# Performance work log

Hardware: AMD Instinct MI355X
Metric: run time of the kernel (lower is better)

## Reference

```python
import jax, jax.numpy as jnp
import numpy as np

S, B, V = 128, 64, 32000
EH, EO, H, O = 512, 512, 1024, 1024
THRESH = 1e-06


def _thresh(x):
    # nn.Threshold(1e-6, 0): x if x > 1e-6 else 0
    return jnp.where(x > THRESH, x, 0.0)


def setup_inputs() -> dict:
    key = jax.random.key(0)
    ks = jax.random.split(key, 12)
    ids = jax.random.randint(ks[0], (S, B), 0, V, dtype=jnp.int32)
    s = 0.02
    return {
        "ids": ids,
        "W1": jax.random.normal(ks[1], (EH, V), jnp.float32) * s,
        "b1": jax.random.normal(ks[2], (EH,), jnp.float32) * s,
        "W2": jax.random.normal(ks[3], (EO, EH), jnp.float32) * s,
        "b2": jax.random.normal(ks[4], (EO,), jnp.float32) * s,
        "W_ih": jax.random.normal(ks[5], (3 * H, EO), jnp.float32) * s,
        "b_ih": jax.random.normal(ks[6], (3 * H,), jnp.float32) * s,
        "W_hh": jax.random.normal(ks[7], (3 * H, H), jnp.float32) * s,
        "b_hh": jax.random.normal(ks[8], (3 * H,), jnp.float32) * s,
        "W_out": jax.random.normal(ks[9], (O, H), jnp.float32) * s,
        "b_out": jax.random.normal(ks[10], (O,), jnp.float32) * s,
    }


def reference(ids, W1, b1, W2, b2, W_ih, b_ih, W_hh, b_hh, W_out, b_out):
    # one_hot(ids, V) @ W1.T + b1 == exact gather of W1 columns (sum of zeros is exact)
    emb = _thresh(jnp.take(W1.T, ids, axis=0) + b1)            # [S, B, EH]
    x = _thresh(jnp.einsum('sbe,oe->sbo', emb, W2) + b2)       # [S, B, EO]
    # Precompute all input-gate projections in one GEMM
    xW = jnp.einsum('sbe,ge->sbg', x, W_ih) + b_ih             # [S, B, 3H]

    def step(h, xw):
        gh = h @ W_hh.T + b_hh                                 # [B, 3H]
        xr, xz, xn = jnp.split(xw, 3, axis=-1)
        hr, hz, hn = jnp.split(gh, 3, axis=-1)
        r = jax.nn.sigmoid(xr + hr)
        z = jax.nn.sigmoid(xz + hz)
        n = jnp.tanh(xn + r * hn)
        h_new = (1.0 - z) * n + z * h
        return h_new, None

    h0 = jnp.zeros((B, H), dtype=x.dtype)
    hT, _ = jax.lax.scan(step, h0, xW)                         # [B, H]
    # Dropout is identity in inference; final Linear
    out = hT @ W_out.T + b_out                                 # [B, O]
    return out[None]                                           # [1, B, O] (h_n layout)
```

## Files before the change

### kernel.cpp

```cpp
#include <hip/hip_runtime.h>
#include <stdint.h>
#include <stddef.h>

#define S_LEN 128
#define B_SZ  64
#define V_SZ  32000
#define EH    512
#define EO    512
#define H_SZ  1024
#define O_SZ  1024
#define G3    3072

typedef __attribute__((ext_vector_type(8))) short short8;
typedef __attribute__((ext_vector_type(4))) float floatx4;
typedef __attribute__((ext_vector_type(8))) unsigned short ushortx8;
typedef __attribute__((ext_vector_type(4))) unsigned uintx4;

__device__ __forceinline__ unsigned short f2bf(float f) {
  unsigned u = __builtin_bit_cast(unsigned, f);
  u += 0x7FFFu + ((u >> 16) & 1u);
  return (unsigned short)(u >> 16);
}
__device__ __forceinline__ float bf2f(unsigned short h) {
  unsigned u = ((unsigned)h) << 16;
  return __builtin_bit_cast(float, u);
}

__device__ __forceinline__ void gld_lds16(const void* g, void* l) {
  __builtin_amdgcn_global_load_lds((const __attribute__((address_space(1))) void*)g,
                                   (__attribute__((address_space(3))) void*)l, 16, 0, 0);
}

__global__ __launch_bounds__(256) void cvt_bf16(const float* __restrict__ in,
                                                unsigned short* __restrict__ out, int n4) {
  int i = blockIdx.x * 256 + threadIdx.x;
  if (i < n4) {
    float4 v = ((const float4*)in)[i];
    ushort4 o;
    o.x = f2bf(v.x); o.y = f2bf(v.y); o.z = f2bf(v.z); o.w = f2bf(v.w);
    ((ushort4*)out)[i] = o;
  }
}

__global__ __launch_bounds__(256) void transpose_w1_bf16(const float* __restrict__ W1,
                                                         unsigned short* __restrict__ W1T) {
  __shared__ unsigned short tile[64][72];
  int t = threadIdx.x;
  int v0 = blockIdx.x * 64;
  int e0 = blockIdx.y * 64;
  for (int i = 0; i < 4; ++i) {
    int e = (t >> 4) + i * 16;
    int v = (t & 15) * 4;
    float4 w = *(const float4*)&W1[(size_t)(e0 + e) * V_SZ + v0 + v];
    tile[v + 0][e] = f2bf(w.x);
    tile[v + 1][e] = f2bf(w.y);
    tile[v + 2][e] = f2bf(w.z);
    tile[v + 3][e] = f2bf(w.w);
  }
  __syncthreads();
  for (int i = 0; i < 2; ++i) {
    int v = (t >> 3) + i * 32;
    int e = (t & 7) * 8;
    ushortx8 o;
    for (int j = 0; j < 8; ++j) o[j] = tile[v][e + j];
    *(ushortx8*)&W1T[(size_t)(v0 + v) * EH + e0 + e] = o;
  }
}

__global__ __launch_bounds__(256) void gather_emb(const int* __restrict__ ids,
                                                  const unsigned short* __restrict__ W1T,
                                                  const float* __restrict__ b1,
                                                  unsigned short* __restrict__ emb) {
  int t = threadIdx.x;
  int tok = blockIdx.x * 4 + (t >> 6);
  int lane = t & 63;
  int id = ids[tok];
  ushortx8 w = *(const ushortx8*)&W1T[(size_t)id * EH + lane * 8];
  float4 blo = *(const float4*)&b1[lane * 8];
  float4 bhi = *(const float4*)&b1[lane * 8 + 4];
  float bv[8] = {blo.x, blo.y, blo.z, blo.w, bhi.x, bhi.y, bhi.z, bhi.w};
  ushortx8 o;
  for (int j = 0; j < 8; ++j) {
    float x = bf2f(w[j]) + bv[j];
    x = (x > 1e-6f) ? x : 0.0f;
    o[j] = f2bf(x);
  }
  *(ushortx8*)&emb[(size_t)tok * EH + lane * 8] = o;
}

template <int ACT, int OUT_BF16>
__global__ __launch_bounds__(256) void gemm_bt(const unsigned short* __restrict__ A,
                                               const unsigned short* __restrict__ B,
                                               const float* __restrict__ bias,
                                               void* __restrict__ Cout,
                                               int M, int N, int K) {
  __shared__ unsigned short lA[128 * 32];
  __shared__ unsigned short lB[128 * 32];
  int t = threadIdx.x;
  int lane = t & 63;
  int wave = t >> 6;
  int bn = blockIdx.x, bm = blockIdx.y;
  int wm = (wave >> 1) * 64;
  int wn = (wave & 1) * 64;
  floatx4 acc[4][4] = {};

  int arow = t >> 2;
  int acol = (t & 3) * 8;

  int ga0 = bm * 128 + arow;       if (ga0 >= M) ga0 = M - 1;
  int ga1 = bm * 128 + arow + 64;  if (ga1 >= M) ga1 = M - 1;
  const unsigned short* a0 = A + (size_t)ga0 * K + acol;
  const unsigned short* a1 = A + (size_t)ga1 * K + acol;
  const unsigned short* b0 = B + (size_t)(bn * 128 + arow) * K + acol;
  const unsigned short* b1 = B + (size_t)(bn * 128 + arow + 64) * K + acol;
  unsigned short* lA0 = &lA[t * 8];
  unsigned short* lA1 = &lA[t * 8 + 64 * 32];
  unsigned short* lB0 = &lB[t * 8];
  unsigned short* lB1 = &lB[t * 8 + 64 * 32];

  for (int k0 = 0; k0 < K; k0 += 32) {
    __syncthreads();
    gld_lds16(a0 + k0, lA0);
    gld_lds16(a1 + k0, lA1);
    gld_lds16(b0 + k0, lB0);
    gld_lds16(b1 + k0, lB1);
    __syncthreads();
    short8 af[4], bfr[4];
    for (int i = 0; i < 4; ++i)
      af[i] = *(const short8*)&lA[(wm + i * 16 + (lane & 15)) * 32 + (lane >> 4) * 8];
    for (int j = 0; j < 4; ++j)
      bfr[j] = *(const short8*)&lB[(wn + j * 16 + (lane & 15)) * 32 + (lane >> 4) * 8];
    for (int i = 0; i < 4; ++i)
      for (int j = 0; j < 4; ++j)
        acc[i][j] = __builtin_amdgcn_mfma_f32_16x16x32_bf16(af[i], bfr[j], acc[i][j], 0, 0, 0);
  }

  int rowq = (lane >> 4) * 4;
  for (int j = 0; j < 4; ++j) {
    int col = bn * 128 + wn + j * 16 + (lane & 15);
    float bv = bias[col];
    for (int i = 0; i < 4; ++i) {
      int row0 = bm * 128 + wm + i * 16 + rowq;
      for (int r = 0; r < 4; ++r) {
        int row = row0 + r;
        if (row < M) {
          float v = acc[i][j][r] + bv;
          if (ACT) v = (v > 1e-6f) ? v : 0.0f;
          if (OUT_BF16) ((unsigned short*)Cout)[(size_t)row * N + col] = f2bf(v);
          else          ((float*)Cout)[(size_t)row * N + col] = v;
        }
      }
    }
  }
}

__global__ __launch_bounds__(256) void prep_whh(const float* __restrict__ W_hh,
                                                unsigned short* __restrict__ Wprep) {
  int tid = blockIdx.x * 256 + threadIdx.x;
  int lane = tid & 63;
  int c = tid >> 6;
  int cg = c / 96;
  int r  = c % 96;
  int g  = r >> 5;
  int t  = r & 31;
  int row = g * H_SZ + cg * 16 + (lane & 15);
  int k   = t * 32 + (lane >> 4) * 8;
  const float* src = &W_hh[(size_t)row * H_SZ + k];
  float4 v0 = *(const float4*)src;
  float4 v1 = *(const float4*)(src + 4);
  ushortx8 o;
  o[0] = f2bf(v0.x); o[1] = f2bf(v0.y); o[2] = f2bf(v0.z); o[3] = f2bf(v0.w);
  o[4] = f2bf(v1.x); o[5] = f2bf(v1.y); o[6] = f2bf(v1.z); o[7] = f2bf(v1.w);
  ((ushortx8*)Wprep)[tid] = o;
}

__global__ __launch_bounds__(256) void gru_persist(const unsigned short* __restrict__ hprep0,
                                                   unsigned short* __restrict__ hprep1,
                                                   unsigned short* __restrict__ hbfinal,
                                                   const unsigned short* __restrict__ Wprep,
                                                   const float* __restrict__ b_hh,
                                                   const unsigned short* __restrict__ xW,
                                                   unsigned* __restrict__ bar) {
  __shared__ unsigned short lB[96 * 512];
  __shared__ float lgh[3][4][256];
  __shared__ float lhf[256];
  int t = threadIdx.x;
  int lane = t & 63;
  int w = t >> 6;
  int bg = blockIdx.x >> 6;
  int cg = blockIdx.x & 63;

  const unsigned short* wsrc = Wprep + (size_t)cg * 96 * 512;
  for (int i = 0; i < 24; ++i) {
    int c = w * 24 + i;
    gld_lds16(wsrc + (size_t)c * 512 + lane * 8, &lB[c * 512 + lane * 8]);
  }
  lhf[t] = 0.0f;

  int b_loc = t >> 4;
  int j_loc = t & 15;
  int jcol = cg * 16 + j_loc;
  int bglob = bg * 16 + b_loc;
  float bhr = b_hh[jcol];
  float bhz = b_hh[H_SZ + jcol];
  float bhn = b_hh[2 * H_SZ + jcol];
  int tt2 = jcol >> 5;
  int q   = (jcol >> 3) & 3;
  int jj  = jcol & 7;
  int Ls  = b_loc | (q << 4);
  size_t hw_off32 = ((((size_t)(bg * 32 + tt2) * 64 + Ls) * 8) + (jj & ~1)) >> 1;

  const unsigned short* hbufs[2] = {hprep0, hprep1};
  unsigned* barp = bar + bg * 64;
  __syncthreads();

  for (int s = 0; s < S_LEN; ++s) {
    const unsigned short* hr = hbufs[s & 1];
    unsigned* hw32 = (unsigned*)hbufs[(s + 1) & 1];

    uintx4 av[8];
#pragma unroll
    for (int i = 0; i < 8; ++i) {
      int tt = w * 8 + i;
      const void* ap = hr + ((size_t)(bg * 32 + tt) * 64 + lane) * 8;
      asm volatile("global_load_dwordx4 %0, %1, off sc1" : "=v"(av[i]) : "v"(ap));
    }
    const unsigned short* xs = xW + (size_t)s * B_SZ * G3 + (size_t)bglob * G3;
    float xr = bf2f(xs[jcol]);
    float xz = bf2f(xs[H_SZ + jcol]);
    float xn = bf2f(xs[2 * H_SZ + jcol]);
    asm volatile("s_waitcnt vmcnt(0)"
                 : "+v"(av[0]), "+v"(av[1]), "+v"(av[2]), "+v"(av[3]),
                   "+v"(av[4]), "+v"(av[5]), "+v"(av[6]), "+v"(av[7])
                 :: "memory");

    floatx4 acc[3] = {};
#pragma unroll
    for (int i = 0; i < 8; ++i) {
      int tt = w * 8 + i;
      short8 a = __builtin_bit_cast(short8, av[i]);
#pragma unroll
      for (int g = 0; g < 3; ++g) {
        short8 bfr = *(const short8*)&lB[((g * 32 + tt) * 64 + lane) * 8];
        acc[g] = __builtin_amdgcn_mfma_f32_16x16x32_bf16(a, bfr, acc[g], 0, 0, 0);
      }
    }
#pragma unroll
    for (int g = 0; g < 3; ++g)
#pragma unroll
      for (int r = 0; r < 4; ++r)
        lgh[g][w][((lane >> 4) * 4 + r) * 16 + (lane & 15)] = acc[g][r];
    __syncthreads();

    float ghr = lgh[0][0][t] + lgh[0][1][t] + lgh[0][2][t] + lgh[0][3][t] + bhr;
    float ghz = lgh[1][0][t] + lgh[1][1][t] + lgh[1][2][t] + lgh[1][3][t] + bhz;
    float ghn = lgh[2][0][t] + lgh[2][1][t] + lgh[2][2][t] + lgh[2][3][t] + bhn;
    float rr = 1.0f / (1.0f + __expf(-(xr + ghr)));
    float zz = 1.0f / (1.0f + __expf(-(xz + ghz)));
    float nn = tanhf(xn + rr * ghn);
    float ho = lhf[t];
    float hnew = (1.0f - zz) * nn + zz * ho;
    lhf[t] = hnew;

    unsigned hb = (unsigned)f2bf(hnew);
    unsigned other = (unsigned)__shfl_xor((int)hb, 1);
    if ((jj & 1) == 0) {
      unsigned packed = hb | (other << 16);
      __hip_atomic_store(hw32 + hw_off32, packed,
                         __ATOMIC_RELAXED, __HIP_MEMORY_SCOPE_AGENT);
    }
    if (s == S_LEN - 1) hbfinal[(size_t)bglob * H_SZ + jcol] = (unsigned short)hb;

    if (s < S_LEN - 1) {
      __syncthreads();
      if (t == 0) {
        __hip_atomic_fetch_add(barp, 1u, __ATOMIC_RELAXED, __HIP_MEMORY_SCOPE_AGENT);
        unsigned target = 64u * (unsigned)(s + 1);
        while (__hip_atomic_load(barp, __ATOMIC_RELAXED, __HIP_MEMORY_SCOPE_AGENT) < target)
          __builtin_amdgcn_s_sleep(2);
      }
      __syncthreads();
    }
  }
}

extern "C" void kernel_launch(void* const* d_in, const int* in_sizes, int n_in,
                              void* d_out, int out_size, void* d_ws, size_t ws_size,
                              hipStream_t stream) {
  const int*   ids   = (const int*)d_in[0];
  const float* W1    = (const float*)d_in[1];
  const float* b1    = (const float*)d_in[2];
  const float* W2    = (const float*)d_in[3];
  const float* b2    = (const float*)d_in[4];
  const float* W_ih  = (const float*)d_in[5];
  const float* b_ih  = (const float*)d_in[6];
  const float* W_hh  = (const float*)d_in[7];
  const float* b_hh  = (const float*)d_in[8];
  const float* W_out = (const float*)d_in[9];
  const float* b_out = (const float*)d_in[10];
  float* out = (float*)d_out;

  uint8_t* wsp = (uint8_t*)d_ws;
  auto alloc = [&](size_t bytes) {
    uint8_t* p = wsp;
    wsp += (bytes + 255) & ~(size_t)255;
    return p;
  };
  unsigned short* W1T   = (unsigned short*)alloc((size_t)V_SZ * EH * 2);
  unsigned short* W2b   = (unsigned short*)alloc((size_t)EO * EH * 2);
  unsigned short* Wihb  = (unsigned short*)alloc((size_t)G3 * EO * 2);
  unsigned short* Wprep = (unsigned short*)alloc((size_t)G3 * H_SZ * 2);
  unsigned short* Woutb = (unsigned short*)alloc((size_t)O_SZ * H_SZ * 2);
  unsigned short* emb   = (unsigned short*)alloc((size_t)S_LEN * B_SZ * EH * 2);
  unsigned short* x     = (unsigned short*)alloc((size_t)S_LEN * B_SZ * EO * 2);
  unsigned short* xW    = (unsigned short*)alloc((size_t)S_LEN * B_SZ * G3 * 2);
  unsigned short* hprep0 = (unsigned short*)alloc((size_t)B_SZ * H_SZ * 2);
  unsigned short* hprep1 = (unsigned short*)alloc((size_t)B_SZ * H_SZ * 2);
  unsigned short* hbfinal = (unsigned short*)alloc((size_t)B_SZ * H_SZ * 2);
  unsigned*       bar     = (unsigned*)alloc(1024);

  {
    int n4;
    n4 = (EO * EH) / 4;
    cvt_bf16<<<dim3((n4 + 255) / 256), 256, 0, stream>>>(W2, W2b, n4);
    n4 = (G3 * EO) / 4;
    cvt_bf16<<<dim3((n4 + 255) / 256), 256, 0, stream>>>(W_ih, Wihb, n4);
    n4 = (O_SZ * H_SZ) / 4;
    cvt_bf16<<<dim3((n4 + 255) / 256), 256, 0, stream>>>(W_out, Woutb, n4);
  }
  prep_whh<<<dim3(1536), 256, 0, stream>>>(W_hh, Wprep);

  hipMemsetAsync(hprep0, 0, (size_t)B_SZ * H_SZ * 2, stream);
  hipMemsetAsync(bar, 0, 1024, stream);

  transpose_w1_bf16<<<dim3(V_SZ / 64, EH / 64), 256, 0, stream>>>(W1, W1T);

  gather_emb<<<dim3(S_LEN * B_SZ / 4), 256, 0, stream>>>(ids, W1T, b1, emb);

  gemm_bt<1, 1><<<dim3(EO / 128, S_LEN * B_SZ / 128), 256, 0, stream>>>(
      emb, W2b, b2, x, S_LEN * B_SZ, EO, EH);

  gemm_bt<0, 1><<<dim3(G3 / 128, S_LEN * B_SZ / 128), 256, 0, stream>>>(
      x, Wihb, b_ih, xW, S_LEN * B_SZ, G3, EO);

  {
    void* args[] = {(void*)&hprep0, (void*)&hprep1, (void*)&hbfinal,
                    (void*)&Wprep, (void*)&b_hh, (void*)&xW, (void*)&bar};
    hipLaunchCooperativeKernel((const void*)gru_persist, dim3(256), dim3(256),
                               args, 0, stream);
  }

  gemm_bt<0, 0><<<dim3(O_SZ / 128, 1), 256, 0, stream>>>(
      hbfinal, Woutb, b_out, out, B_SZ, O_SZ, H_SZ);
}
```

Before: 663.1 us.

## Replace GRU atomic counter barrier with per-wave flag polling and fuse weight conversions

The persistent GRU kernel drops the counter barrier (one atomic add plus a sleep-poll by thread 0, bracketed by two __syncthreads) in favour of per-wave step flags. Each wave publishes its step number and then polls the 64 flags of its batch group, one per lane, with no block-level syncs; the lgh scratch is double-buffered by step parity so there is no reuse hazard. The hidden state is kept in a register instead of LDS, and the three weight-conversion launches are merged into one kernel over a contiguous output buffer. The risks are heavier flag traffic from busy polling with no sleep, and relaxed-ordering correctness that depends on s_waitcnt before each flag store.

Measured after the change: 869.3 us. +31.1%, slower.

```diff
diff --git a/kernel.cpp b/kernel.cpp
--- a/kernel.cpp
+++ b/kernel.cpp
@@ -31,15 +31,22 @@
                                    (__attribute__((address_space(3))) void*)l, 16, 0, 0);
 }
 
-__global__ __launch_bounds__(256) void cvt_bf16(const float* __restrict__ in,
-                                                unsigned short* __restrict__ out, int n4) {
+__global__ __launch_bounds__(256) void cvt3_bf16(const float* __restrict__ a,
+                                                 const float* __restrict__ b,
+                                                 const float* __restrict__ c,
+                                                 unsigned short* __restrict__ out) {
+  const int na4 = (EO * EH) / 4;
+  const int nb4 = (G3 * EO) / 4;
   int i = blockIdx.x * 256 + threadIdx.x;
-  if (i < n4) {
-    float4 v = ((const float4*)in)[i];
-    ushort4 o;
-    o.x = f2bf(v.x); o.y = f2bf(v.y); o.z = f2bf(v.z); o.w = f2bf(v.w);
-    ((ushort4*)out)[i] = o;
-  }
+  const float* src;
+  int off;
+  if (i < na4)            { src = a; off = i; }
+  else if (i < na4 + nb4) { src = b; off = i - na4; }
+  else                    { src = c; off = i - na4 - nb4; }
+  float4 v = ((const float4*)src)[off];
+  ushort4 o;
+  o.x = f2bf(v.x); o.y = f2bf(v.y); o.z = f2bf(v.z); o.w = f2bf(v.w);
+  ((ushort4*)out)[i] = o;
 }
 
 __global__ __launch_bounds__(256) void transpose_w1_bf16(const float* __restrict__ W1,
@@ -180,10 +187,9 @@
                                                    const unsigned short* __restrict__ Wprep,
                                                    const float* __restrict__ b_hh,
                                                    const unsigned short* __restrict__ xW,
-                                                   unsigned* __restrict__ bar) {
+                                                   unsigned* __restrict__ flags) {
   __shared__ unsigned short lB[96 * 512];
-  __shared__ float lgh[3][4][256];
-  __shared__ float lhf[256];
+  __shared__ float lgh[2][3][4][256];
   int t = threadIdx.x;
   int lane = t & 63;
   int w = t >> 6;
@@ -195,7 +201,6 @@
     int c = w * 24 + i;
     gld_lds16(wsrc + (size_t)c * 512 + lane * 8, &lB[c * 512 + lane * 8]);
   }
-  lhf[t] = 0.0f;
 
   int b_loc = t >> 4;
   int j_loc = t & 15;
@@ -210,8 +215,11 @@
   int Ls  = b_loc | (q << 4);
   size_t hw_off32 = ((((size_t)(bg * 32 + tt2) * 64 + Ls) * 8) + (jj & ~1)) >> 1;
 
+  unsigned* fstore = flags + bg * 256 + cg * 4 + w;
+  const unsigned* fpoll = flags + bg * 256 + w * 64 + lane;
+
+  float hmaster = 0.0f;
   const unsigned short* hbufs[2] = {hprep0, hprep1};
-  unsigned* barp = bar + bg * 64;
   __syncthreads();
 
   for (int s = 0; s < S_LEN; ++s) {
@@ -245,22 +253,22 @@
         acc[g] = __builtin_amdgcn_mfma_f32_16x16x32_bf16(a, bfr, acc[g], 0, 0, 0);
       }
     }
+    int par = s & 1;
 #pragma unroll
     for (int g = 0; g < 3; ++g)
 #pragma unroll
       for (int r = 0; r < 4; ++r)
-        lgh[g][w][((lane >> 4) * 4 + r) * 16 + (lane & 15)] = acc[g][r];
+        lgh[par][g][w][((lane >> 4) * 4 + r) * 16 + (lane & 15)] = acc[g][r];
     __syncthreads();
 
-    float ghr = lgh[0][0][t] + lgh[0][1][t] + lgh[0][2][t] + lgh[0][3][t] + bhr;
-    float ghz = lgh[1][0][t] + lgh[1][1][t] + lgh[1][2][t] + lgh[1][3][t] + bhz;
-    float ghn = lgh[2][0][t] + lgh[2][1][t] + lgh[2][2][t] + lgh[2][3][t] + bhn;
+    float ghr = lgh[par][0][0][t] + lgh[par][0][1][t] + lgh[par][0][2][t] + lgh[par][0][3][t] + bhr;
+    float ghz = lgh[par][1][0][t] + lgh[par][1][1][t] + lgh[par][1][2][t] + lgh[par][1][3][t] + bhz;
+    float ghn = lgh[par][2][0][t] + lgh[par][2][1][t] + lgh[par][2][2][t] + lgh[par][2][3][t] + bhn;
     float rr = 1.0f / (1.0f + __expf(-(xr + ghr)));
     float zz = 1.0f / (1.0f + __expf(-(xz + ghz)));
     float nn = tanhf(xn + rr * ghn);
-    float ho = lhf[t];
-    float hnew = (1.0f - zz) * nn + zz * ho;
-    lhf[t] = hnew;
+    float hnew = (1.0f - zz) * nn + zz * hmaster;
+    hmaster = hnew;
 
     unsigned hb = (unsigned)f2bf(hnew);
     unsigned other = (unsigned)__shfl_xor((int)hb, 1);
@@ -269,17 +277,17 @@
       __hip_atomic_store(hw32 + hw_off32, packed,
                          __ATOMIC_RELAXED, __HIP_MEMORY_SCOPE_AGENT);
     }
-    if (s == S_LEN - 1) hbfinal[(size_t)bglob * H_SZ + jcol] = (unsigned short)hb;
-
-    if (s < S_LEN - 1) {
-      __syncthreads();
-      if (t == 0) {
-        __hip_atomic_fetch_add(barp, 1u, __ATOMIC_RELAXED, __HIP_MEMORY_SCOPE_AGENT);
-        unsigned target = 64u * (unsigned)(s + 1);
-        while (__hip_atomic_load(barp, __ATOMIC_RELAXED, __HIP_MEMORY_SCOPE_AGENT) < target)
-          __builtin_amdgcn_s_sleep(2);
-      }
-      __syncthreads();
+
+    if (s == S_LEN - 1) {
+      hbfinal[(size_t)bglob * H_SZ + jcol] = (unsigned short)hb;
+    } else {
+      asm volatile("s_waitcnt vmcnt(0)" ::: "memory");
+      if (lane == 0)
+        __hip_atomic_store(fstore, (unsigned)(s + 1),
+                           __ATOMIC_RELAXED, __HIP_MEMORY_SCOPE_AGENT);
+      unsigned tgt = (unsigned)(s + 1);
+      while (__hip_atomic_load(fpoll, __ATOMIC_RELAXED,
+                               __HIP_MEMORY_SCOPE_AGENT) < tgt) {}
     }
   }
 }
@@ -309,29 +317,22 @@
   unsigned short* W1T   = (unsigned short*)alloc((size_t)V_SZ * EH * 2);
   unsigned short* W2b   = (unsigned short*)alloc((size_t)EO * EH * 2);
   unsigned short* Wihb  = (unsigned short*)alloc((size_t)G3 * EO * 2);
+  unsigned short* Woutb = (unsigned short*)alloc((size_t)O_SZ * H_SZ * 2);
   unsigned short* Wprep = (unsigned short*)alloc((size_t)G3 * H_SZ * 2);
-  unsigned short* Woutb = (unsigned short*)alloc((size_t)O_SZ * H_SZ * 2);
   unsigned short* emb   = (unsigned short*)alloc((size_t)S_LEN * B_SZ * EH * 2);
   unsigned short* x     = (unsigned short*)alloc((size_t)S_LEN * B_SZ * EO * 2);
   unsigned short* xW    = (unsigned short*)alloc((size_t)S_LEN * B_SZ * G3 * 2);
   unsigned short* hprep0 = (unsigned short*)alloc((size_t)B_SZ * H_SZ * 2);
   unsigned short* hprep1 = (unsigned short*)alloc((size_t)B_SZ * H_SZ * 2);
   unsigned short* hbfinal = (unsigned short*)alloc((size_t)B_SZ * H_SZ * 2);
-  unsigned*       bar     = (unsigned*)alloc(1024);
-
-  {
-    int n4;
-    n4 = (EO * EH) / 4;
-    cvt_bf16<<<dim3((n4 + 255) / 256), 256, 0, stream>>>(W2, W2b, n4);
-    n4 = (G3 * EO) / 4;
-    cvt_bf16<<<dim3((n4 + 255) / 256), 256, 0, stream>>>(W_ih, Wihb, n4);
-    n4 = (O_SZ * H_SZ) / 4;
-    cvt_bf16<<<dim3((n4 + 255) / 256), 256, 0, stream>>>(W_out, Woutb, n4);
-  }
+  unsigned*       flags   = (unsigned*)alloc(4096);
+
+  cvt3_bf16<<<dim3(2816), 256, 0, stream>>>(W2, W_ih, W_out, W2b);
+
   prep_whh<<<dim3(1536), 256, 0, stream>>>(W_hh, Wprep);
 
   hipMemsetAsync(hprep0, 0, (size_t)B_SZ * H_SZ * 2, stream);
-  hipMemsetAsync(bar, 0, 1024, stream);
+  hipMemsetAsync(flags, 0, 4096, stream);
 
   transpose_w1_bf16<<<dim3(V_SZ / 64, EH / 64), 256, 0, stream>>>(W1, W1T);
 
@@ -345,7 +346,7 @@
 
   {
     void* args[] = {(void*)&hprep0, (void*)&hprep1, (void*)&hbfinal,
-                    (void*)&Wprep, (void*)&b_hh, (void*)&xW, (void*)&bar};
+                    (void*)&Wprep, (void*)&b_hh, (void*)&xW, (void*)&flags};
     hipLaunchCooperativeKernel((const void*)gru_persist, dim3(256), dim3(256),
                                args, 0, stream);
   }
```

## Merge weight conversions into one launch and widen GEMM K-tile with swizzled LDS

Applied to the files above, without the earlier changes.

Replaces three separate fp32-to-bf16 conversion launches with a single kernel that writes into contiguous buffers, with Woutb reordered so it follows Wihb in memory. The bf16 GEMM now stages 64-wide K slices instead of 32, using an XOR-swizzled LDS layout to avoid bank conflicts. Each tile runs two MFMA sub-steps per barrier pair, which cuts barrier count and launch overhead. It also doubles LDS use per block and relies on the contiguous buffer layout staying aligned (256-byte allocation rounding holds for these sizes).

New measurement: 652.5 us. Within noise of the previous version (-1.6%).

```diff
diff --git a/kernel.cpp b/kernel.cpp
--- a/kernel.cpp
+++ b/kernel.cpp
@@ -31,15 +31,22 @@
                                    (__attribute__((address_space(3))) void*)l, 16, 0, 0);
 }
 
-__global__ __launch_bounds__(256) void cvt_bf16(const float* __restrict__ in,
-                                                unsigned short* __restrict__ out, int n4) {
+__global__ __launch_bounds__(256) void cvt3_bf16(const float* __restrict__ a,
+                                                 const float* __restrict__ b,
+                                                 const float* __restrict__ c,
+                                                 unsigned short* __restrict__ out) {
+  const int na4 = (EO * EH) / 4;
+  const int nb4 = (G3 * EO) / 4;
   int i = blockIdx.x * 256 + threadIdx.x;
-  if (i < n4) {
-    float4 v = ((const float4*)in)[i];
-    ushort4 o;
-    o.x = f2bf(v.x); o.y = f2bf(v.y); o.z = f2bf(v.z); o.w = f2bf(v.w);
-    ((ushort4*)out)[i] = o;
-  }
+  const float* src;
+  int off;
+  if (i < na4)            { src = a; off = i; }
+  else if (i < na4 + nb4) { src = b; off = i - na4; }
+  else                    { src = c; off = i - na4 - nb4; }
+  float4 v = ((const float4*)src)[off];
+  ushort4 o;
+  o.x = f2bf(v.x); o.y = f2bf(v.y); o.z = f2bf(v.z); o.w = f2bf(v.w);
+  ((ushort4*)out)[i] = o;
 }
 
 __global__ __launch_bounds__(256) void transpose_w1_bf16(const float* __restrict__ W1,
@@ -94,8 +101,8 @@
                                                const float* __restrict__ bias,
                                                void* __restrict__ Cout,
                                                int M, int N, int K) {
-  __shared__ unsigned short lA[128 * 32];
-  __shared__ unsigned short lB[128 * 32];
+  __shared__ unsigned short lA[128 * 64];
+  __shared__ unsigned short lB[128 * 64];
   int t = threadIdx.x;
   int lane = t & 63;
   int wave = t >> 6;
@@ -104,35 +111,48 @@
   int wn = (wave & 1) * 64;
   floatx4 acc[4][4] = {};
 
-  int arow = t >> 2;
-  int acol = (t & 3) * 8;
-
-  int ga0 = bm * 128 + arow;       if (ga0 >= M) ga0 = M - 1;
-  int ga1 = bm * 128 + arow + 64;  if (ga1 >= M) ga1 = M - 1;
-  const unsigned short* a0 = A + (size_t)ga0 * K + acol;
-  const unsigned short* a1 = A + (size_t)ga1 * K + acol;
-  const unsigned short* b0 = B + (size_t)(bn * 128 + arow) * K + acol;
-  const unsigned short* b1 = B + (size_t)(bn * 128 + arow + 64) * K + acol;
-  unsigned short* lA0 = &lA[t * 8];
-  unsigned short* lA1 = &lA[t * 8 + 64 * 32];
-  unsigned short* lB0 = &lB[t * 8];
-  unsigned short* lB1 = &lB[t * 8 + 64 * 32];
-
-  for (int k0 = 0; k0 < K; k0 += 32) {
+  int srow = t >> 3;
+  int sslot = (t & 7) ^ (srow & 7);
+  int scol = sslot * 8;
+
+  const unsigned short* aptr[4];
+  const unsigned short* bptr[4];
+#pragma unroll
+  for (int p = 0; p < 4; ++p) {
+    int gra = bm * 128 + p * 32 + srow;  if (gra >= M) gra = M - 1;
+    aptr[p] = A + (size_t)gra * K + scol;
+    bptr[p] = B + (size_t)(bn * 128 + p * 32 + srow) * K + scol;
+  }
+
+  for (int k0 = 0; k0 < K; k0 += 64) {
     __syncthreads();
-    gld_lds16(a0 + k0, lA0);
-    gld_lds16(a1 + k0, lA1);
-    gld_lds16(b0 + k0, lB0);
-    gld_lds16(b1 + k0, lB1);
+#pragma unroll
+    for (int p = 0; p < 4; ++p) {
+      gld_lds16(aptr[p] + k0, &lA[p * 2048 + t * 8]);
+      gld_lds16(bptr[p] + k0, &lB[p * 2048 + t * 8]);
+    }
     __syncthreads();
-    short8 af[4], bfr[4];
-    for (int i = 0; i < 4; ++i)
-      af[i] = *(const short8*)&lA[(wm + i * 16 + (lane & 15)) * 32 + (lane >> 4) * 8];
-    for (int j = 0; j < 4; ++j)
-      bfr[j] = *(const short8*)&lB[(wn + j * 16 + (lane & 15)) * 32 + (lane >> 4) * 8];
-    for (int i = 0; i < 4; ++i)
-      for (int j = 0; j < 4; ++j)
-        acc[i][j] = __builtin_amdgcn_mfma_f32_16x16x32_bf16(af[i], bfr[j], acc[i][j], 0, 0, 0);
+#pragma unroll
+    for (int kk = 0; kk < 2; ++kk) {
+      short8 af[4], bfr[4];
+#pragma unroll
+      for (int i = 0; i < 4; ++i) {
+        int row = wm + i * 16 + (lane & 15);
+        int phys = (kk * 4 + (lane >> 4)) ^ (row & 7);
+        af[i] = *(const short8*)&lA[row * 64 + phys * 8];
+      }
+#pragma unroll
+      for (int j = 0; j < 4; ++j) {
+        int row = wn + j * 16 + (lane & 15);
+        int phys = (kk * 4 + (lane >> 4)) ^ (row & 7);
+        bfr[j] = *(const short8*)&lB[row * 64 + phys * 8];
+      }
+#pragma unroll
+      for (int i = 0; i < 4; ++i)
+#pragma unroll
+        for (int j = 0; j < 4; ++j)
+          acc[i][j] = __builtin_amdgcn_mfma_f32_16x16x32_bf16(af[i], bfr[j], acc[i][j], 0, 0, 0);
+    }
   }
 
   int rowq = (lane >> 4) * 4;
@@ -309,8 +329,8 @@
   unsigned short* W1T   = (unsigned short*)alloc((size_t)V_SZ * EH * 2);
   unsigned short* W2b   = (unsigned short*)alloc((size_t)EO * EH * 2);
   unsigned short* Wihb  = (unsigned short*)alloc((size_t)G3 * EO * 2);
+  unsigned short* Woutb = (unsigned short*)alloc((size_t)O_SZ * H_SZ * 2);
   unsigned short* Wprep = (unsigned short*)alloc((size_t)G3 * H_SZ * 2);
-  unsigned short* Woutb = (unsigned short*)alloc((size_t)O_SZ * H_SZ * 2);
   unsigned short* emb   = (unsigned short*)alloc((size_t)S_LEN * B_SZ * EH * 2);
   unsigned short* x     = (unsigned short*)alloc((size_t)S_LEN * B_SZ * EO * 2);
   unsigned short* xW    = (unsigned short*)alloc((size_t)S_LEN * B_SZ * G3 * 2);
@@ -319,15 +339,8 @@
   unsigned short* hbfinal = (unsigned short*)alloc((size_t)B_SZ * H_SZ * 2);
   unsigned*       bar     = (unsigned*)alloc(1024);
 
-  {
-    int n4;
-    n4 = (EO * EH) / 4;
-    cvt_bf16<<<dim3((n4 + 255) / 256), 256, 0, stream>>>(W2, W2b, n4);
-    n4 = (G3 * EO) / 4;
-    cvt_bf16<<<dim3((n4 + 255) / 256), 256, 0, stream>>>(W_ih, Wihb, n4);
-    n4 = (O_SZ * H_SZ) / 4;
-    cvt_bf16<<<dim3((n4 + 255) / 256), 256, 0, stream>>>(W_out, Woutb, n4);
-  }
+  cvt3_bf16<<<dim3(2816), 256, 0, stream>>>(W2, W_ih, W_out, W2b);
+
   prep_whh<<<dim3(1536), 256, 0, stream>>>(W_hh, Wprep);
 
   hipMemsetAsync(hprep0, 0, (size_t)B_SZ * H_SZ * 2, stream);
```
